# Kernel tuning notes

Hardware: AMD Instinct MI355X
Metric: run time of the kernel (lower is better)

The kernel has to match this reference:

```python
import jax, jax.numpy as jnp
import numpy as np

M_QAM = 16
LEAD_SYMBOLS = 20000  # pilot prefix in 'test' mode
NSYMB = 40000
NMODES = 256


def qam_constellation(M):
    # square M-QAM grid, normalized to unit average energy (constellation / sqrt(Es))
    m = int(np.sqrt(M))
    levels = 2 * np.arange(m) - (m - 1)
    c = (levels[:, None] + 1j * levels[None, :]).ravel()
    Es = np.mean(np.abs(c) ** 2)
    return (c / np.sqrt(Es)).astype(np.complex64)  # [M]


def setup_inputs() -> dict:
    key = jax.random.key(0)
    k = jax.random.split(key, 4)
    return {
        "Ei_real": jax.random.normal(k[0], (NSYMB, NMODES), jnp.float32),
        "Ei_imag": jax.random.normal(k[1], (NSYMB, NMODES), jnp.float32),
        "tx_real": jax.random.normal(k[2], (NSYMB, NMODES), jnp.float32),
        "tx_imag": jax.random.normal(k[3], (NSYMB, NMODES), jnp.float32),
        "eta": jnp.full((1,), 0.1, jnp.float32),  # learnable 'ddpll eta' param
    }


def _ddpll(Ei, symbTx, Kv, constSymb, mode):
    # k0,k1,k2 = 2*tanh(arctanh(0.5)), 2*tanh(arctanh(-0.5)), 2*tanh(arctanh(0.5))
    k0, k1, k2 = 1.0, -1.0, 1.0

    def Lk(phi, y, target, m):
        z = y * jnp.exp(1j * phi)
        dec = jnp.min(jnp.abs(z - constSymb) ** 2)  # decision-directed (min over M points)
        pil = jnp.abs(z - target) ** 2              # pilot-aided
        return dec * m + pil * (1.0 - m)

    g = jax.vmap(jax.grad(Lk, argnums=0))  # per-mode d Lk / d phi

    def step(carry, data):
        u, phi = carry                 # u: [3, Nmodes], phi: [Nmodes]
        xk, yk, mk = data              # [Nmodes] each
        gk = g(phi, yk, xk, mk)
        u1 = u[2]                      # u[1] <- old u[2]
        u0 = k0 * u[0] + k1 * u1 + k2 * gk  # momentum filter output
        new_u = jnp.stack([u0, u1, gk])
        return (new_u, phi - Kv * u0), phi  # emit pre-update phase (phip)

    Nmodes = Ei.shape[1]
    carry0 = (jnp.zeros((3, Nmodes), jnp.float32), jnp.zeros((Nmodes,), jnp.float32))
    _, theta = jax.lax.scan(step, carry0, (symbTx, Ei, mode))
    theta = jnp.unwrap(theta, axis=0, period=np.pi / 2)
    return Ei * jnp.exp(1j * theta), theta


def reference(Ei_real, Ei_imag, tx_real, tx_imag, eta):
    Ei = Ei_real + 1j * Ei_imag          # [Nsymb, Nmodes] complex64
    symbTx = tx_real + 1j * tx_imag
    Kv = jnp.tanh(eta[0])                # lr = tanh(eta)
    # mode: 0 on pilot rows (first lead_symbols in 'test' mode), 1 elsewhere
    mode = jnp.ones((NSYMB, NMODES), jnp.float32).at[:LEAD_SYMBOLS].set(0.0)
    constSymb = jnp.asarray(qam_constellation(M_QAM))
    Eo, theta = _ddpll(Ei, symbTx, Kv, constSymb, mode)
    return jnp.stack([Eo.real, Eo.imag], axis=-1), theta  # [Nsymb, Nmodes, 2], [Nsymb, Nmodes]
```

## Files before the change

### kernel.cpp

```cpp
#include <hip/hip_runtime.h>
#include <math.h>

#define NSYMB  40000
#define NMODES 256
#define LEAD   20000
#define UF     8
#define NM     (NSYMB * NMODES)

static __device__ __forceinline__ float crhypotf(float a, float b) {
    const double da = (double)a, db = (double)b;
    return (float)sqrt(da * da + db * db);
}

static __device__ __forceinline__ float fmod_p2_exact(float xf) {
    const double y  = (double)1.57079632679489661923f;
    const double ry = 1.0 / ((double)1.57079632679489661923f);
    const double ax = fabs((double)xf);
    const double q  = __builtin_trunc(ax * ry);
    double r = __builtin_fma(-q, y, ax);
    r = (r < 0.0) ? (r + y) : ((r >= y) ? (r - y) : r);
    return copysignf((float)r, xf);
}

static __device__ __forceinline__ void cr_sincosf_nb(double x, float& sf, float& cf) {
    const double invpio2 = 6.36619772367581382433e-01;
    const double pio2_1  = 1.57079632673412561417e+00;
    const double pio2_1t = 6.07710050650619224932e-11;
    const double fn = __builtin_rint(x * invpio2);
    const double rr = __builtin_fma(-fn, pio2_1, x);
    const double yy = rr - fn * pio2_1t;
    const double z  = yy * yy;
    double ps = __builtin_fma(z, 1.58969099521155010221e-10, -2.50507602534068634195e-08);
    ps = __builtin_fma(z, ps,  2.75573137070700676789e-06);
    ps = __builtin_fma(z, ps, -1.98412698298579493134e-04);
    ps = __builtin_fma(z, ps,  8.33333333332248946124e-03);
    ps = __builtin_fma(z, ps, -1.66666666666666324348e-01);
    const double sv = __builtin_fma(yy * z, ps, yy);
    double pc = __builtin_fma(z, -1.13596475577881948265e-11, 2.08757232129817482790e-09);
    pc = __builtin_fma(z, pc, -2.75573143513906633035e-07);
    pc = __builtin_fma(z, pc,  2.48015872894767294178e-05);
    pc = __builtin_fma(z, pc, -1.38888888888741095749e-03);
    pc = __builtin_fma(z, pc,  4.16666666666666019037e-02);
    const double hz = 0.5 * z;
    const double w1 = 1.0 - hz;
    const double cv = w1 + (((1.0 - w1) - hz) + z * (z * pc));
    const int n = ((int)fn) & 3;
    const float S = (float)sv, C = (float)cv;
    const bool sw = (n & 1) != 0;
    const float sa = sw ? C : S;
    const float ca = sw ? S : C;
    sf = (n & 2) ? -sa : sa;
    cf = ((n + 1) & 2) ? -ca : ca;
}

static __device__ __attribute__((noinline)) float2 dd_slow(float zre, float zim) {
#pragma clang fp contract(off)
    const double s10 = sqrt(10.0);
    float Lf[4];
    Lf[0] = (float)(-3.0 / s10); Lf[1] = (float)(-1.0 / s10);
    Lf[2] = (float)( 1.0 / s10); Lf[3] = (float)( 3.0 / s10);
    float dv[16], rv[16], wres[16], wims[16];
    float dmin = __builtin_inff();
#pragma unroll
    for (int k = 0; k < 16; ++k) {
        const float wre = zre - Lf[k >> 2];
        const float wim = zim - Lf[k & 3];
        const float r = crhypotf(wre, wim);
        const float d = r * r;
        wres[k] = wre; wims[k] = wim; rv[k] = r; dv[k] = d;
        dmin = fminf(dmin, d);
    }
    int cnt = 0;
#pragma unroll
    for (int k = 0; k < 16; ++k) cnt += (dv[k] == dmin) ? 1 : 0;
    float A, B;
    if (cnt == 1) {
        int j = 0;
#pragma unroll
        for (int k = 0; k < 16; ++k) if (dv[k] == dmin) j = k;
        A = 2.0f * wres[j];
        B = -(2.0f * wims[j]);
    } else {
        const float ctd = 1.0f / (float)cnt;
        float sa = 0.0f, sb = 0.0f;
#pragma unroll
        for (int k = 0; k < 16; ++k) {
            if (dv[k] == dmin) {
                const float ctr  = (2.0f * rv[k]) * ctd;
                const float ctm2 = ctr / rv[k];
                sa += (ctm2 * wres[k]);
                sb += -(ctm2 * wims[k]);
            }
        }
        A = sa; B = sb;
    }
    return make_float2(A, B);
}

template<bool PILOT>
static __device__ __forceinline__ void phi_step(
    float yre, float yim, float txr, float txi,
    float Kv, const float* Lf, float& phi)
{
#pragma clang fp contract(off)
    const float QTHf = 0.63245553203367588f;
    float s, c;
    cr_sincosf_nb((double)phi, s, c);
    const float zre = (yre * c) - (yim * s);
    const float zim = (yre * s) + (yim * c);
    float A, B;
    if (PILOT) {
        const float wre = zre - txr;
        const float wim = zim - txi;
        A = 2.0f * wre;
        B = -(2.0f * wim);
    } else {
        const float tr = (zre < 0.0f) ? ((zre < -QTHf) ? Lf[0] : Lf[1])
                                      : ((zre <  QTHf) ? Lf[2] : Lf[3]);
        const float ti = (zim < 0.0f) ? ((zim < -QTHf) ? Lf[0] : Lf[1])
                                      : ((zim <  QTHf) ? Lf[2] : Lf[3]);
        const float wre0 = zre - tr;
        const float wim0 = zim - ti;
        A = 2.0f * wre0;
        B = -(2.0f * wim0);
        const float ar = fabsf(zre), ai = fabsf(zim);
        const float mr = fminf(fabsf(ar - QTHf), ar);
        const float mi = fminf(fabsf(ai - QTHf), ai);
        const bool slow = !(mr > 1e-4f && mi > 1e-4f);
        if (__builtin_expect(__ballot(slow) != 0ULL, 0)) {
            if (slow) { const float2 ab = dd_slow(zre, zim); A = ab.x; B = ab.y; }
        }
    }
    const float ct_e_re = (A * yre) - (B * yim);
    const float ct_e_im = (A * yim) + (B * yre);
    const float ct_v_im = (ct_e_re * s) + (ct_e_im * c);
    const float gk = -ct_v_im;
    phi = phi - (Kv * gk);
}

__global__ __launch_bounds__(64)
void ddpll_seq(const float* __restrict__ ei_re,
               const float* __restrict__ ei_im,
               const float* __restrict__ tx_re,
               const float* __restrict__ tx_im,
               const float* __restrict__ eta,
               float* __restrict__ out)
{
#pragma clang fp contract(off)
    const int m = blockIdx.x * 64 + threadIdx.x;
    const float Kv = (float)tanh((double)eta[0]);

    const double s10 = sqrt(10.0);
    float Lf[4];
    Lf[0] = (float)(-3.0 / s10); Lf[1] = (float)(-1.0 / s10);
    Lf[2] = (float)( 1.0 / s10); Lf[3] = (float)( 3.0 / s10);

    float phi = 0.0f;
    float* __restrict__ th_p = out + (size_t)m * NSYMB;

    float pyr[UF], pyi[UF], pxr[UF], pxi[UF];
#pragma unroll
    for (int j = 0; j < UF; ++j) {
        const int idx = j * NMODES + m;
        pyr[j] = ei_re[idx]; pyi[j] = ei_im[idx];
        pxr[j] = tx_re[idx]; pxi[j] = tx_im[idx];
    }
    for (int tb = 0; tb < LEAD; tb += UF) {
        float yr[UF], yi[UF], xr[UF], xi[UF];
#pragma unroll
        for (int j = 0; j < UF; ++j) { yr[j]=pyr[j]; yi[j]=pyi[j]; xr[j]=pxr[j]; xi[j]=pxi[j]; }
        const int nb = tb + UF;
#pragma unroll
        for (int j = 0; j < UF; ++j) {
            const int idx = (nb + j) * NMODES + m;
            pyr[j] = ei_re[idx]; pyi[j] = ei_im[idx];
            pxr[j] = tx_re[idx]; pxi[j] = tx_im[idx];
        }
#pragma unroll
        for (int j = 0; j < UF; ++j) {
            th_p[tb + j] = phi;
            phi_step<true>(yr[j], yi[j], xr[j], xi[j], Kv, Lf, phi);
        }
    }

#pragma unroll
    for (int j = 0; j < UF; ++j) {
        const int idx = (LEAD + j) * NMODES + m;
        pyr[j] = ei_re[idx]; pyi[j] = ei_im[idx];
    }
    for (int tb = LEAD; tb < NSYMB; tb += UF) {
        float yr[UF], yi[UF];
#pragma unroll
        for (int j = 0; j < UF; ++j) { yr[j]=pyr[j]; yi[j]=pyi[j]; }
        const int nb = tb + UF;
#pragma unroll
        for (int j = 0; j < UF; ++j) {
            const int tt = (nb + j < NSYMB) ? (nb + j) : (NSYMB - 1);
            const int idx = tt * NMODES + m;
            pyr[j] = ei_re[idx]; pyi[j] = ei_im[idx];
        }
#pragma unroll
        for (int j = 0; j < UF; ++j) {
            th_p[tb + j] = phi;
            phi_step<false>(yr[j], yi[j], 0.0f, 0.0f, Kv, Lf, phi);
        }
    }
}

__global__ __launch_bounds__(256)
void ddpll_unwrapc(const float* __restrict__ thT, float* __restrict__ cT)
{
#pragma clang fp contract(off)
    const float P2f = 1.57079632679489661923f;
    const float P4f = 0.78539816339744830961f;
    const int g = blockIdx.x * 256 + threadIdx.x;
    const int m = g / NSYMB;
    const int t = g - m * NSYMB;
    float cv = 0.0f;
    if (t > 0) {
        const float thv  = thT[g];
        const float prev = thT[g - 1];
        const float dd = thv - prev;
        float rm = fmod_p2_exact(dd + P4f);
        rm = (rm < 0.0f) ? rm + P2f : rm;
        float ddmod = rm - P4f;
        ddmod = (ddmod == -P4f && dd > 0.0f) ? P4f : ddmod;
        const bool take = !(fabsf(dd) < P4f);
        cv = take ? (ddmod - dd) : 0.0f;
    }
    cT[g] = cv;
}

__global__ __launch_bounds__(64)
void ddpll_scan(const float* __restrict__ thT, const float* __restrict__ cT,
                float* __restrict__ theta)
{
#pragma clang fp contract(off)
    const int m = blockIdx.x * 64 + threadIdx.x;
    const float4* __restrict__ pth = (const float4*)(thT + (size_t)m * NSYMB);
    const float4* __restrict__ pcv = (const float4*)(cT  + (size_t)m * NSYMB);
    float cum = 0.0f;
    float4 bth[8], bcv[8];
#pragma unroll
    for (int j = 0; j < 8; ++j) { bth[j] = pth[j]; bcv[j] = pcv[j]; }
    for (int tb = 0; tb < NSYMB; tb += 32) {
        float4 th_[8], cv_[8];
#pragma unroll
        for (int j = 0; j < 8; ++j) { th_[j] = bth[j]; cv_[j] = bcv[j]; }
        const int nb4 = (tb + 32) >> 2;
#pragma unroll
        for (int j = 0; j < 8; ++j) { bth[j] = pth[nb4 + j]; bcv[j] = pcv[nb4 + j]; }
#pragma unroll
        for (int j = 0; j < 8; ++j) {
#pragma unroll
            for (int k = 0; k < 4; ++k) {
                const float cc = (&cv_[j].x)[k];
                const float tt = (&th_[j].x)[k];
                cum = cum + cc;
                theta[(tb + j * 4 + k) * NMODES + m] = tt + cum;
            }
        }
    }
}

__global__ __launch_bounds__(256)
void ddpll_rot(const float* __restrict__ ei_re,
               const float* __restrict__ ei_im,
               float* __restrict__ out)
{
    const int idx = blockIdx.x * 256 + threadIdx.x;
    const float U = out[(size_t)2 * NM + idx];
    float su, cu;
    sincosf(U, &su, &cu);
    const float yre = ei_re[idx], yim = ei_im[idx];
    out[2 * idx]     = (yre * cu) - (yim * su);
    out[2 * idx + 1] = (yre * su) + (yim * cu);
}

extern "C" void kernel_launch(void* const* d_in, const int* in_sizes, int n_in,
                              void* d_out, int out_size, void* d_ws, size_t ws_size,
                              hipStream_t stream)
{
    (void)in_sizes; (void)n_in; (void)out_size; (void)d_ws; (void)ws_size;
    const float* ei_re = (const float*)d_in[0];
    const float* ei_im = (const float*)d_in[1];
    float* out = (float*)d_out;
    float* thT = out;
    float* cT  = out + (size_t)NM;
    float* th  = out + (size_t)2 * NM;

    ddpll_seq<<<dim3(NMODES / 64), dim3(64), 0, stream>>>(
        ei_re, ei_im,
        (const float*)d_in[2],
        (const float*)d_in[3],
        (const float*)d_in[4],
        out);
    ddpll_unwrapc<<<dim3(NM / 256), dim3(256), 0, stream>>>(thT, cT);
    ddpll_scan<<<dim3(NMODES / 64), dim3(64), 0, stream>>>(thT, cT, th);
    ddpll_rot<<<dim3(NM / 256), dim3(256), 0, stream>>>(ei_re, ei_im, out);
}
```

Measured before the change: 11.88 ms.

## Process two independent modes per thread to interleave serial PLL chains

Each thread of the sequential PLL kernel now advances two independent mode recurrences (m and m+128) in lockstep, and the kernel launches 2 blocks instead of 4. The aim is to hide the latency of the long serial dependency chain (double-precision sincos, decision logic) through instruction-level parallelism between the two chains. The unroll/prefetch depth drops from 8 to 4 to limit register pressure. The trade-off is that half as many waves run on separate compute units, so each wave does twice the work and the result depends on whether the latency-bound chain gets overlapped.

```diff
diff --git a/kernel.cpp b/kernel.cpp
--- a/kernel.cpp
+++ b/kernel.cpp
@@ -4,7 +4,7 @@
 #define NSYMB  40000
 #define NMODES 256
 #define LEAD   20000
-#define UF     8
+#define UF     4
 #define NM     (NSYMB * NMODES)
 
 static __device__ __forceinline__ float crhypotf(float a, float b) {
@@ -98,44 +98,64 @@
 }
 
 template<bool PILOT>
-static __device__ __forceinline__ void phi_step(
-    float yre, float yim, float txr, float txi,
-    float Kv, const float* Lf, float& phi)
+static __device__ __forceinline__ void pll2_step(
+    float yreA, float yimA, float txrA, float txiA,
+    float yreB, float yimB, float txrB, float txiB,
+    float Kv, const float* Lf, float& phiA, float& phiB)
 {
 #pragma clang fp contract(off)
     const float QTHf = 0.63245553203367588f;
-    float s, c;
-    cr_sincosf_nb((double)phi, s, c);
-    const float zre = (yre * c) - (yim * s);
-    const float zim = (yre * s) + (yim * c);
-    float A, B;
+    float sA, cA, sB, cB;
+    cr_sincosf_nb((double)phiA, sA, cA);
+    cr_sincosf_nb((double)phiB, sB, cB);
+    const float zreA = (yreA * cA) - (yimA * sA);
+    const float zimA = (yreA * sA) + (yimA * cA);
+    const float zreB = (yreB * cB) - (yimB * sB);
+    const float zimB = (yreB * sB) + (yimB * cB);
+    float AA, BA, AB, BB;
     if (PILOT) {
-        const float wre = zre - txr;
-        const float wim = zim - txi;
-        A = 2.0f * wre;
-        B = -(2.0f * wim);
+        const float wreA = zreA - txrA;
+        const float wimA = zimA - txiA;
+        AA = 2.0f * wreA;
+        BA = -(2.0f * wimA);
+        const float wreB = zreB - txrB;
+        const float wimB = zimB - txiB;
+        AB = 2.0f * wreB;
+        BB = -(2.0f * wimB);
     } else {
-        const float tr = (zre < 0.0f) ? ((zre < -QTHf) ? Lf[0] : Lf[1])
-                                      : ((zre <  QTHf) ? Lf[2] : Lf[3]);
-        const float ti = (zim < 0.0f) ? ((zim < -QTHf) ? Lf[0] : Lf[1])
-                                      : ((zim <  QTHf) ? Lf[2] : Lf[3]);
-        const float wre0 = zre - tr;
-        const float wim0 = zim - ti;
-        A = 2.0f * wre0;
-        B = -(2.0f * wim0);
-        const float ar = fabsf(zre), ai = fabsf(zim);
-        const float mr = fminf(fabsf(ar - QTHf), ar);
-        const float mi = fminf(fabsf(ai - QTHf), ai);
-        const bool slow = !(mr > 1e-4f && mi > 1e-4f);
-        if (__builtin_expect(__ballot(slow) != 0ULL, 0)) {
-            if (slow) { const float2 ab = dd_slow(zre, zim); A = ab.x; B = ab.y; }
-        }
-    }
-    const float ct_e_re = (A * yre) - (B * yim);
-    const float ct_e_im = (A * yim) + (B * yre);
-    const float ct_v_im = (ct_e_re * s) + (ct_e_im * c);
-    const float gk = -ct_v_im;
-    phi = phi - (Kv * gk);
+        const float trA = (zreA < 0.0f) ? ((zreA < -QTHf) ? Lf[0] : Lf[1])
+                                        : ((zreA <  QTHf) ? Lf[2] : Lf[3]);
+        const float tiA = (zimA < 0.0f) ? ((zimA < -QTHf) ? Lf[0] : Lf[1])
+                                        : ((zimA <  QTHf) ? Lf[2] : Lf[3]);
+        AA = 2.0f * (zreA - trA);
+        BA = -(2.0f * (zimA - tiA));
+        const float trB = (zreB < 0.0f) ? ((zreB < -QTHf) ? Lf[0] : Lf[1])
+                                        : ((zreB <  QTHf) ? Lf[2] : Lf[3]);
+        const float tiB = (zimB < 0.0f) ? ((zimB < -QTHf) ? Lf[0] : Lf[1])
+                                        : ((zimB <  QTHf) ? Lf[2] : Lf[3]);
+        AB = 2.0f * (zreB - trB);
+        BB = -(2.0f * (zimB - tiB));
+        const float arA = fabsf(zreA), aiA = fabsf(zimA);
+        const float mrA = fminf(fabsf(arA - QTHf), arA);
+        const float miA = fminf(fabsf(aiA - QTHf), aiA);
+        const bool slowA = !(mrA > 1e-4f && miA > 1e-4f);
+        const float arB = fabsf(zreB), aiB = fabsf(zimB);
+        const float mrB = fminf(fabsf(arB - QTHf), arB);
+        const float miB = fminf(fabsf(aiB - QTHf), aiB);
+        const bool slowB = !(mrB > 1e-4f && miB > 1e-4f);
+        if (__builtin_expect(__ballot(slowA || slowB) != 0ULL, 0)) {
+            if (slowA) { const float2 ab = dd_slow(zreA, zimA); AA = ab.x; BA = ab.y; }
+            if (slowB) { const float2 ab = dd_slow(zreB, zimB); AB = ab.x; BB = ab.y; }
+        }
+    }
+    const float ct_e_reA = (AA * yreA) - (BA * yimA);
+    const float ct_e_imA = (AA * yimA) + (BA * yreA);
+    const float ct_v_imA = (ct_e_reA * sA) + (ct_e_imA * cA);
+    phiA = phiA - (Kv * (-ct_v_imA));
+    const float ct_e_reB = (AB * yreB) - (BB * yimB);
+    const float ct_e_imB = (AB * yimB) + (BB * yreB);
+    const float ct_v_imB = (ct_e_reB * sB) + (ct_e_imB * cB);
+    phiB = phiB - (Kv * (-ct_v_imB));
 }
 
 __global__ __launch_bounds__(64)
@@ -147,7 +167,8 @@
                float* __restrict__ out)
 {
 #pragma clang fp contract(off)
-    const int m = blockIdx.x * 64 + threadIdx.x;
+    const int mA = blockIdx.x * 64 + threadIdx.x;
+    const int mB = mA + 128;
     const float Kv = (float)tanh((double)eta[0]);
 
     const double s10 = sqrt(10.0);
@@ -155,54 +176,78 @@
     Lf[0] = (float)(-3.0 / s10); Lf[1] = (float)(-1.0 / s10);
     Lf[2] = (float)( 1.0 / s10); Lf[3] = (float)( 3.0 / s10);
 
-    float phi = 0.0f;
-    float* __restrict__ th_p = out + (size_t)m * NSYMB;
-
-    float pyr[UF], pyi[UF], pxr[UF], pxi[UF];
+    float phiA = 0.0f, phiB = 0.0f;
+    float* __restrict__ thA = out + (size_t)mA * NSYMB;
+    float* __restrict__ thB = out + (size_t)mB * NSYMB;
+
+    float ayr[UF], ayi[UF], axr[UF], axi[UF];
+    float byr[UF], byi[UF], bxr[UF], bxi[UF];
+    float Pay[UF], Pai[UF], Par[UF], Pax[UF];
+    float Pby[UF], Pbi[UF], Pbr[UF], Pbx[UF];
 #pragma unroll
     for (int j = 0; j < UF; ++j) {
-        const int idx = j * NMODES + m;
-        pyr[j] = ei_re[idx]; pyi[j] = ei_im[idx];
-        pxr[j] = tx_re[idx]; pxi[j] = tx_im[idx];
+        const int ia = j * NMODES + mA;
+        const int ib = j * NMODES + mB;
+        Pay[j] = ei_re[ia]; Pai[j] = ei_im[ia];
+        Par[j] = tx_re[ia]; Pax[j] = tx_im[ia];
+        Pby[j] = ei_re[ib]; Pbi[j] = ei_im[ib];
+        Pbr[j] = tx_re[ib]; Pbx[j] = tx_im[ib];
     }
     for (int tb = 0; tb < LEAD; tb += UF) {
-        float yr[UF], yi[UF], xr[UF], xi[UF];
-#pragma unroll
-        for (int j = 0; j < UF; ++j) { yr[j]=pyr[j]; yi[j]=pyi[j]; xr[j]=pxr[j]; xi[j]=pxi[j]; }
+#pragma unroll
+        for (int j = 0; j < UF; ++j) {
+            ayr[j]=Pay[j]; ayi[j]=Pai[j]; axr[j]=Par[j]; axi[j]=Pax[j];
+            byr[j]=Pby[j]; byi[j]=Pbi[j]; bxr[j]=Pbr[j]; bxi[j]=Pbx[j];
+        }
         const int nb = tb + UF;
 #pragma unroll
         for (int j = 0; j < UF; ++j) {
-            const int idx = (nb + j) * NMODES + m;
-            pyr[j] = ei_re[idx]; pyi[j] = ei_im[idx];
-            pxr[j] = tx_re[idx]; pxi[j] = tx_im[idx];
-        }
-#pragma unroll
-        for (int j = 0; j < UF; ++j) {
-            th_p[tb + j] = phi;
-            phi_step<true>(yr[j], yi[j], xr[j], xi[j], Kv, Lf, phi);
+            const int ia = (nb + j) * NMODES + mA;
+            const int ib = (nb + j) * NMODES + mB;
+            Pay[j] = ei_re[ia]; Pai[j] = ei_im[ia];
+            Par[j] = tx_re[ia]; Pax[j] = tx_im[ia];
+            Pby[j] = ei_re[ib]; Pbi[j] = ei_im[ib];
+            Pbr[j] = tx_re[ib]; Pbx[j] = tx_im[ib];
+        }
+#pragma unroll
+        for (int j = 0; j < UF; ++j) {
+            thA[tb + j] = phiA;
+            thB[tb + j] = phiB;
+            pll2_step<true>(ayr[j], ayi[j], axr[j], axi[j],
+                            byr[j], byi[j], bxr[j], bxi[j],
+                            Kv, Lf, phiA, phiB);
         }
     }
 
 #pragma unroll
     for (int j = 0; j < UF; ++j) {
-        const int idx = (LEAD + j) * NMODES + m;
-        pyr[j] = ei_re[idx]; pyi[j] = ei_im[idx];
+        const int ia = (LEAD + j) * NMODES + mA;
+        const int ib = (LEAD + j) * NMODES + mB;
+        Pay[j] = ei_re[ia]; Pai[j] = ei_im[ia];
+        Pby[j] = ei_re[ib]; Pbi[j] = ei_im[ib];
     }
     for (int tb = LEAD; tb < NSYMB; tb += UF) {
-        float yr[UF], yi[UF];
-#pragma unroll
-        for (int j = 0; j < UF; ++j) { yr[j]=pyr[j]; yi[j]=pyi[j]; }
+#pragma unroll
+        for (int j = 0; j < UF; ++j) {
+            ayr[j]=Pay[j]; ayi[j]=Pai[j];
+            byr[j]=Pby[j]; byi[j]=Pbi[j];
+        }
         const int nb = tb + UF;
 #pragma unroll
         for (int j = 0; j < UF; ++j) {
             const int tt = (nb + j < NSYMB) ? (nb + j) : (NSYMB - 1);
-            const int idx = tt * NMODES + m;
-            pyr[j] = ei_re[idx]; pyi[j] = ei_im[idx];
-        }
-#pragma unroll
-        for (int j = 0; j < UF; ++j) {
-            th_p[tb + j] = phi;
-            phi_step<false>(yr[j], yi[j], 0.0f, 0.0f, Kv, Lf, phi);
+            const int ia = tt * NMODES + mA;
+            const int ib = tt * NMODES + mB;
+            Pay[j] = ei_re[ia]; Pai[j] = ei_im[ia];
+            Pby[j] = ei_re[ib]; Pbi[j] = ei_im[ib];
+        }
+#pragma unroll
+        for (int j = 0; j < UF; ++j) {
+            thA[tb + j] = phiA;
+            thB[tb + j] = phiB;
+            pll2_step<false>(ayr[j], ayi[j], 0.0f, 0.0f,
+                             byr[j], byi[j], 0.0f, 0.0f,
+                             Kv, Lf, phiA, phiB);
         }
     }
 }
@@ -289,7 +334,7 @@
     float* cT  = out + (size_t)NM;
     float* th  = out + (size_t)2 * NM;
 
-    ddpll_seq<<<dim3(NMODES / 64), dim3(64), 0, stream>>>(
+    ddpll_seq<<<dim3(2), dim3(64), 0, stream>>>(
         ei_re, ei_im,
         (const float*)d_in[2],
         (const float*)d_in[3],
```

Result: slower. 19.71 ms (+65.9%).
